# Optimization experiments

Hardware: AMD Instinct MI355X
Metric: run time of the kernel (lower is better)

Reference implementation:

```python
import jax, jax.numpy as jnp
import numpy as np

HID = 256; HEADS = 8; HD = HID // HEADS; GROUPS = 8; CPG = HID // GROUPS
DIMS = [64, 128, 256, 512]; SIZES = [56, 28, 14, 7]; B = 8


def _linear(x, W, b):
    # torch nn.Linear convention: W is [out, in]
    return jnp.einsum('...i,oi->...o', x, W) + b


def _conv1x1(x, W, b):
    return jnp.einsum('bchw,oc->bohw', x, W) + b[None, :, None, None]


def setup_inputs() -> dict:
    key = jax.random.key(0)
    keys = iter(jax.random.split(key, 64))
    def nrm(shape, s=0.02):
        return jax.random.normal(next(keys), shape, dtype=jnp.float32) * s
    inp = {}
    for i, (d, sz) in enumerate(zip(DIMS, SIZES)):
        inp[f'f{i}'] = jax.random.normal(next(keys), (B, d, sz, sz), dtype=jnp.float32)
        inp[f'Wp{i}'] = nrm((HID, d)); inp[f'bp{i}'] = jnp.zeros((HID,), jnp.float32)
    for n, shp in [('Wq', (HID, HID)), ('Wk', (HID, HID)), ('Wv', (HID, HID)), ('Wo', (HID, HID)),
                   ('Wg1', (HID, 2 * HID)), ('Wg2', (HID, HID)), ('Wcp', (HID, HID)),
                   ('Wkg1', (2 * HID, HID)), ('Wkg2', (GROUPS * 9, 2 * HID)),
                   ('Wit', (HID, HID)), ('Wot', (HID, HID))]:
        inp[n] = nrm(shp)
    for n, dim in [('bq', HID), ('bk', HID), ('bv', HID), ('bo', HID), ('bg1', HID), ('bg2', HID),
                   ('bcp', HID), ('bkg1', 2 * HID), ('bkg2', GROUPS * 9), ('bit', HID), ('bot', HID)]:
        inp[n] = jnp.zeros((dim,), jnp.float32)
    inp['gamma'] = jnp.ones((HID,), jnp.float32)
    inp['beta'] = jnp.zeros((HID,), jnp.float32)
    return inp


def reference(f0, f1, f2, f3, Wp0, bp0, Wp1, bp1, Wp2, bp2, Wp3, bp3,
              Wq, bq, Wk, bk, Wv, bv, Wo, bo, Wg1, bg1, Wg2, bg2,
              Wcp, bcp, Wkg1, bkg1, Wkg2, bkg2, Wit, bit, Wot, bot, gamma, beta):
    feats = [f0, f1, f2, f3]
    Wps = [Wp0, Wp1, Wp2, Wp3]; bps = [bp0, bp1, bp2, bp3]
    b = f0.shape[0]
    # ---- ACSA: 1x1 projections to hidden_dim, flatten spatial to tokens ----
    proj = [_conv1x1(f, W, bb) for f, W, bb in zip(feats, Wps, bps)]  # [B,HID,H,W]
    flat = [p.reshape(b, HID, -1).transpose(0, 2, 1) for p in proj]   # [B,S,HID]
    scale = 1.0 / jnp.sqrt(jnp.float32(HD))
    enhanced = []
    for i, xi in enumerate(flat):
        q = _linear(xi, Wq, bq).reshape(b, -1, HEADS, HD).transpose(0, 2, 1, 3)  # [B,H,Si,d]
        e = xi
        for j, xj in enumerate(flat):
            if i == j:
                continue
            k = _linear(xj, Wk, bk).reshape(b, -1, HEADS, HD).transpose(0, 2, 1, 3)
            v = _linear(xj, Wv, bv).reshape(b, -1, HEADS, HD).transpose(0, 2, 1, 3)
            attn = jax.nn.softmax(jnp.einsum('bhqd,bhkd->bhqk', q, k) * scale, axis=-1)
            ctx = jnp.einsum('bhqk,bhkd->bhqd', attn, v).transpose(0, 2, 1, 3).reshape(b, -1, HID)
            ctx = _linear(ctx, Wo, bo)
            gate = jax.nn.sigmoid(_linear(jax.nn.relu(_linear(jnp.concatenate([e, ctx], -1), Wg1, bg1)), Wg2, bg2))
            e = e + gate * ctx
        enhanced.append(e.transpose(0, 2, 1).reshape(b, HID, proj[i].shape[2], proj[i].shape[3]))
    # ---- CECM per scale: dynamic per-sample grouped 3x3 conv ----
    outs = []
    for x in enhanced:
        H, W = x.shape[2], x.shape[3]
        ctx = jax.nn.relu(_linear(x.mean((2, 3)), Wcp, bcp))                       # [B,HID]
        kern = _linear(jax.nn.relu(_linear(ctx, Wkg1, bkg1)), Wkg2, bkg2)          # [B,G*9]
        kern = kern.reshape(b, GROUPS, 3, 3)
        xt = _conv1x1(x, Wit, bit)                                                 # [B,HID,H,W]
        # per-(sample,group) kernel shared across channels within group -> depthwise conv
        kern_rep = jnp.broadcast_to(kern[:, :, None], (b, GROUPS, CPG, 3, 3)).reshape(b * HID, 1, 3, 3)
        y = jax.lax.conv_general_dilated(
            xt.reshape(1, b * HID, H, W), kern_rep, (1, 1), ((1, 1), (1, 1)),
            dimension_numbers=('NCHW', 'OIHW', 'NCHW'), feature_group_count=b * HID
        ).reshape(b, HID, H, W)
        y = _conv1x1(y, Wot, bot)
        # BatchNorm2d (training-mode batch statistics, biased var, eps=1e-5)
        mu = y.mean((0, 2, 3)); var = y.var((0, 2, 3))
        y = (y - mu[None, :, None, None]) * jax.lax.rsqrt(var + 1e-5)[None, :, None, None]
        y = y * gamma[None, :, None, None] + beta[None, :, None, None]
        outs.append((xt + y).reshape(b, HID, -1))
    # concat scales along flattened-spatial axis -> [B, HID, 3136+784+196+49]
    return jnp.concatenate(outs, axis=-1)
```

## Files before the change

### kernel.cpp

```cpp
#include <hip/hip_runtime.h>
#include <hip/hip_bf16.h>
#include <cstddef>

#define NB 8
#define HIDC 256
#define NHEAD 8
#define HDIM 32
#define TTOK 33320
#define STOT 4165
#define VTP 33440
#define QKVS 768
#define QSC2 0.2550348757f
#define BN1_CH 128

static const int H_SZ[4]   = {56, 28, 14, 7};
static const int S_SZ[4]   = {3136, 784, 196, 49};
static const int D_IN[4]   = {64, 128, 256, 512};
static const int BOFF[4]   = {0, 25088, 31360, 32928};
static const int SKPAD_H[4]= {3136, 784, 200, 56};
static const int VWOFF_H[4]= {0, 25088, 31360, 32960};

__constant__ int DC_S[4]     = {3136, 784, 196, 49};
__constant__ int DC_HW[4]    = {56, 28, 14, 7};
__constant__ int DC_BOFF[4]  = {0, 25088, 31360, 32928};
__constant__ int DC_GOFF[4]  = {0, 3136, 3920, 4116};
__constant__ int DC_FOS[4]   = {0, 49, 62, 66};

__constant__ int FP_SQ[12]   = {784,196,49,3136,196,49,3136,784,49,3136,784,196};
__constant__ int FP_SK[12]   = {3136,3136,3136,784,784,784,196,196,196,49,49,49};
__constant__ int FP_QOFF[12] = {25088,31360,32928,0,31360,32928,0,25088,32928,0,25088,31360};
__constant__ int FP_KOFF[12] = {0,0,0,25088,25088,25088,31360,31360,31360,32928,32928,32928};
__constant__ int FP_VOFF[12] = {0,0,0,25088,25088,25088,31360,31360,31360,32960,32960,32960};
__constant__ int FP_SKP[12]  = {3136,3136,3136,784,784,784,200,200,200,56,56,56};
__constant__ int FP_R[12]    = {0,0,0,0,1,1,1,1,2,2,2,2};
__constant__ int FP_SB0[13]  = {0,13,17,18,31,32,33,46,50,51,64,68,69};

typedef short bf16s;
typedef bf16s bf16x8 __attribute__((ext_vector_type(8)));
typedef float f32x4 __attribute__((ext_vector_type(4)));

static __device__ inline bf16s f2b(float f) {
    return (bf16s)((__float_as_uint(f) + 0x8000u) >> 16);
}
static __device__ inline float b2f(bf16s s) {
    return __uint_as_float(((unsigned)(unsigned short)s) << 16);
}
static __device__ inline unsigned cvtpk(float a, float b) {
    unsigned r;
    asm("v_cvt_pk_bf16_f32 %0, %1, %2" : "=v"(r) : "v"(a), "v"(b));
    return r;
}
static __device__ inline float ex2(float x) {
#if __has_builtin(__builtin_amdgcn_exp2f)
    return __builtin_amdgcn_exp2f(x);
#else
    return exp2f(x);
#endif
}
#define MFMA16(a, b, c) __builtin_amdgcn_mfma_f32_16x16x32_bf16(a, b, c, 0, 0, 0)
#define ZERO4 ((f32x4){0.f, 0.f, 0.f, 0.f})

struct CvtArgs {
    const float* src[15];
    void* dst[15];
    int n[15];
    int mode[15];
    int K[15];
};
__global__ __launch_bounds__(256) void cvt_all(CvtArgs a, int total) {
    int idx = blockIdx.x * 256 + threadIdx.x;
    if (idx >= total) return;
    int seg = 0, off = idx;
    while (off >= a.n[seg]) { off -= a.n[seg]; seg++; }
    float v = a.src[seg][off];
    int m = a.mode[seg];
    if (m == 1 || m == 3) v *= QSC2;
    if (m <= 1) {
        int K = a.K[seg];
        int kz = __builtin_ctz(K);
        int n = off >> kz, k = off & (K - 1);
        int c64 = n >> 6, nt = (n >> 4) & 3, l15 = n & 15;
        int k32 = k >> 5, q = (k >> 3) & 3, j = k & 7;
        int dst = (((c64 * (K >> 5) + k32) * 4 + nt) << 9) + l15 * 32 + q * 8 + j;
        ((bf16s*)a.dst[seg])[dst] = f2b(v);
    } else {
        ((float*)a.dst[seg])[off] = v;
    }
}

__global__ __launch_bounds__(256) void transpose_f2(const float* __restrict__ f,
                                                    bf16s* __restrict__ A, int D, int S) {
    __shared__ float t[32][33];
    int s0 = blockIdx.x * 32, d0 = blockIdx.y * 32, b = blockIdx.z;
    int sl = threadIdx.x & 31, dl = threadIdx.x >> 5;
    #pragma unroll
    for (int dd = 0; dd < 32; dd += 8) {
        int s = s0 + sl;
        t[dl + dd][sl] = (s < S) ? f[((size_t)(b * D + d0 + dl + dd)) * S + s] : 0.f;
    }
    __syncthreads();
    int dc = threadIdx.x & 31, sg = threadIdx.x >> 5;
    #pragma unroll
    for (int ss = 0; ss < 32; ss += 8) {
        int s = s0 + sg + ss;
        if (s < S) A[((size_t)(b * S + s)) * D + d0 + dc] = f2b(t[dc][sg + ss]);
    }
}

template <int EPI>
__global__ __launch_bounds__(256) void gemm3(
    const bf16s* __restrict__ A, const bf16s* __restrict__ A2,
    const bf16s* __restrict__ W, const float* __restrict__ bias,
    float* __restrict__ Cf, bf16s* __restrict__ Cb, const bf16s* __restrict__ Gaux,
    int M, int N, int K, int K1)
{
    int tid = threadIdx.x, lane = tid & 63, wave = tid >> 6;
    int l15 = lane & 15, quad = lane >> 4;
    int row0 = blockIdx.y * 64 + (wave >> 1) * 32;
    int col0 = blockIdx.x * 128 + (wave & 1) * 64;
    int K2 = K - K1;
    int nk = K >> 5;
    int c64 = (blockIdx.x << 1) + (wave & 1);
    const bf16s* wbase = W + (size_t)c64 * ((size_t)nk << 11) + l15 * 32 + quad * 8;
    int ra[2];
    #pragma unroll
    for (int mt = 0; mt < 2; mt++) ra[mt] = min(row0 + mt * 16 + l15, M - 1);

    f32x4 acc[2][4];
    #pragma unroll
    for (int i = 0; i < 2; i++)
        #pragma unroll
        for (int j = 0; j < 4; j++) acc[i][j] = ZERO4;

    bf16x8 aA[2], wA[4], aB[2], wB[4];

    auto loadA = [&](bf16x8* af, int k32) {
        int kk = (k32 << 5) + quad * 8;
        if (kk < K1) {
            #pragma unroll
            for (int mt = 0; mt < 2; mt++)
                af[mt] = *(const bf16x8*)(A + (size_t)ra[mt] * K1 + kk);
        } else {
            int k2 = kk - K1;
            #pragma unroll
            for (int mt = 0; mt < 2; mt++)
                af[mt] = *(const bf16x8*)(A2 + (size_t)ra[mt] * K2 + k2);
        }
    };
    auto loadW = [&](bf16x8* wf, int k32) {
        const bf16s* p = wbase + ((size_t)k32 << 11);
        #pragma unroll
        for (int nt = 0; nt < 4; nt++)
            wf[nt] = *(const bf16x8*)(p + nt * 512);
    };

    loadA(aA, 0); loadW(wA, 0);
    for (int k32 = 0; k32 < nk; k32 += 2) {
        loadA(aB, k32 + 1); loadW(wB, k32 + 1);
        #pragma unroll
        for (int mt = 0; mt < 2; mt++)
            #pragma unroll
            for (int nt = 0; nt < 4; nt++)
                acc[mt][nt] = MFMA16(aA[mt], wA[nt], acc[mt][nt]);
        if (k32 + 2 < nk) { loadA(aA, k32 + 2); loadW(wA, k32 + 2); }
        #pragma unroll
        for (int mt = 0; mt < 2; mt++)
            #pragma unroll
            for (int nt = 0; nt < 4; nt++)
                acc[mt][nt] = MFMA16(aB[mt], wB[nt], acc[mt][nt]);
    }

    #pragma unroll
    for (int mt = 0; mt < 2; mt++) {
        int rowb = row0 + mt * 16 + quad * 4;
        #pragma unroll
        for (int nt = 0; nt < 4; nt++) {
            int col = col0 + nt * 16 + l15;
            float bv = bias ? bias[col] : 0.f;
            #pragma unroll
            for (int r = 0; r < 4; r++) {
                int row = rowb + r;
                if (row >= M) continue;
                size_t off = (size_t)row * N + col;
                float v = acc[mt][nt][r] + bv;
                if (EPI == 0) {
                    Cb[off] = f2b(v);
                } else if (EPI == 1) {
                    Cf[off] = v; Cb[off] = f2b(v);
                } else {
                    Cf[off] = v;
                }
            }
        }
    }
}

#define GLDS 264
__global__ __launch_bounds__(256) void gatefuse(
    const bf16s* __restrict__ ctxob, bf16s* __restrict__ xb, const float* __restrict__ x,
    const bf16s* __restrict__ Wg1, const float* __restrict__ bg1,
    const bf16s* __restrict__ Wg2, const float* __restrict__ bg2, int M)
{
    __shared__ bf16s ebf[32 * GLDS], cxb[32 * GLDS], hbf[32 * GLDS];
    int tid = threadIdx.x, lane = tid & 63, wave = tid >> 6;
    int l15 = lane & 15, quad = lane >> 4;
    int r0 = blockIdx.x * 32;
    int col0 = wave * 64;

    #pragma unroll
    for (int u = 0; u < 4; u++) {
        int idx = u * 256 + tid;
        int row = idx >> 5, ch = (idx & 31) * 8;
        *(bf16x8*)&ebf[row * GLDS + ch] =
            *(const bf16x8*)(xb + (size_t)min(r0 + row, M - 1) * HIDC + ch);
    }
    f32x4 e32[2][4];
    #pragma unroll
    for (int mt = 0; mt < 2; mt++)
        #pragma unroll
        for (int nt = 0; nt < 4; nt++)
            #pragma unroll
            for (int rr = 0; rr < 4; rr++) {
                int row = min(r0 + mt * 16 + quad * 4 + rr, M - 1);
                e32[mt][nt][rr] = x[(size_t)row * HIDC + col0 + nt * 16 + l15];
            }

    const bf16s* w1base = Wg1 + ((size_t)wave << 15) + l15 * 32 + quad * 8;
    const bf16s* w2base = Wg2 + ((size_t)wave << 14) + l15 * 32 + quad * 8;

    for (int r = 0; r < 3; r++) {
        __syncthreads();
        const bf16s* crp = ctxob + (size_t)r * ((size_t)TTOK * HIDC);
        #pragma unroll
        for (int u = 0; u < 4; u++) {
            int idx = u * 256 + tid;
            int row = idx >> 5, ch = (idx & 31) * 8;
            *(bf16x8*)&cxb[row * GLDS + ch] =
                *(const bf16x8*)(crp + (size_t)min(r0 + row, M - 1) * HIDC + ch);
        }
        __syncthreads();

        f32x4 acc[2][4];
        bf16x8 aA[2], wA[4], aB[2], wB[4];

        #pragma unroll
        for (int i = 0; i < 2; i++)
            #pragma unroll
            for (int j = 0; j < 4; j++) acc[i][j] = ZERO4;
        auto loadA1 = [&](bf16x8* af, int k32) {
            int kk = (k32 << 5) + quad * 8;
            if (kk < 256) {
                #pragma unroll
                for (int mt = 0; mt < 2; mt++)
                    af[mt] = *(const bf16x8*)&ebf[(mt * 16 + l15) * GLDS + kk];
            } else {
                #pragma unroll
                for (int mt = 0; mt < 2; mt++)
                    af[mt] = *(const bf16x8*)&cxb[(mt * 16 + l15) * GLDS + kk - 256];
            }
        };
        auto loadW1 = [&](bf16x8* wf, int k32) {
            const bf16s* p = w1base + ((size_t)k32 << 11);
            #pragma unroll
            for (int nt = 0; nt < 4; nt++)
                wf[nt] = *(const bf16x8*)(p + nt * 512);
        };
        loadA1(aA, 0); loadW1(wA, 0);
        for (int k32 = 0; k32 < 16; k32 += 2) {
            loadA1(aB, k32 + 1); loadW1(wB, k32 + 1);
            #pragma unroll
            for (int mt = 0; mt < 2; mt++)
                #pragma unroll
                for (int nt = 0; nt < 4; nt++)
                    acc[mt][nt] = MFMA16(aA[mt], wA[nt], acc[mt][nt]);
            if (k32 + 2 < 16) { loadA1(aA, k32 + 2); loadW1(wA, k32 + 2); }
            #pragma unroll
            for (int mt = 0; mt < 2; mt++)
                #pragma unroll
                for (int nt = 0; nt < 4; nt++)
                    acc[mt][nt] = MFMA16(aB[mt], wB[nt], acc[mt][nt]);
        }
        #pragma unroll
        for (int mt = 0; mt < 2; mt++)
            #pragma unroll
            for (int nt = 0; nt < 4; nt++)
                #pragma unroll
                for (int rr = 0; rr < 4; rr++) {
                    int row = mt * 16 + quad * 4 + rr;
                    int col = col0 + nt * 16 + l15;
                    hbf[row * GLDS + col] = f2b(fmaxf(acc[mt][nt][rr] + bg1[col], 0.f));
                }
        __syncthreads();

        #pragma unroll
        for (int i = 0; i < 2; i++)
            #pragma unroll
            for (int j = 0; j < 4; j++) acc[i][j] = ZERO4;
        auto loadA2 = [&](bf16x8* af, int k32) {
            int kk = (k32 << 5) + quad * 8;
            #pragma unroll
            for (int mt = 0; mt < 2; mt++)
                af[mt] = *(const bf16x8*)&hbf[(mt * 16 + l15) * GLDS + kk];
        };
        auto loadW2 = [&](bf16x8* wf, int k32) {
            const bf16s* p = w2base + ((size_t)k32 << 11);
            #pragma unroll
            for (int nt = 0; nt < 4; nt++)
                wf[nt] = *(const bf16x8*)(p + nt * 512);
        };
        loadA2(aA, 0); loadW2(wA, 0);
        for (int k32 = 0; k32 < 8; k32 += 2) {
            loadA2(aB, k32 + 1); loadW2(wB, k32 + 1);
            #pragma unroll
            for (int mt = 0; mt < 2; mt++)
                #pragma unroll
                for (int nt = 0; nt < 4; nt++)
                    acc[mt][nt] = MFMA16(aA[mt], wA[nt], acc[mt][nt]);
            if (k32 + 2 < 8) { loadA2(aA, k32 + 2); loadW2(wA, k32 + 2); }
            #pragma unroll
            for (int mt = 0; mt < 2; mt++)
                #pragma unroll
                for (int nt = 0; nt < 4; nt++)
                    acc[mt][nt] = MFMA16(aB[mt], wB[nt], acc[mt][nt]);
        }
        #pragma unroll
        for (int mt = 0; mt < 2; mt++)
            #pragma unroll
            for (int nt = 0; nt < 4; nt++)
                #pragma unroll
                for (int rr = 0; rr < 4; rr++) {
                    int row = mt * 16 + quad * 4 + rr;
                    int col = col0 + nt * 16 + l15;
                    float v = acc[mt][nt][rr] + bg2[col];
                    float g = 1.f / (1.f + __expf(-v));
                    e32[mt][nt][rr] += g * b2f(cxb[row * GLDS + col]);
                }
        if (r < 2) {
            #pragma unroll
            for (int mt = 0; mt < 2; mt++)
                #pragma unroll
                for (int nt = 0; nt < 4; nt++)
                    #pragma unroll
                    for (int rr = 0; rr < 4; rr++) {
                        int row = mt * 16 + quad * 4 + rr;
                        int col = col0 + nt * 16 + l15;
                        ebf[row * GLDS + col] = f2b(e32[mt][nt][rr]);
                    }
        }
    }

    #pragma unroll
    for (int mt = 0; mt < 2; mt++)
        #pragma unroll
        for (int nt = 0; nt < 4; nt++)
            #pragma unroll
            for (int rr = 0; rr < 4; rr++) {
                int row = r0 + mt * 16 + quad * 4 + rr;
                if (row < M)
                    xb[(size_t)row * HIDC + col0 + nt * 16 + l15] = f2b(e32[mt][nt][rr]);
            }
}

__global__ __launch_bounds__(256) void transpose_v(const bf16s* __restrict__ vsrc,
                                                   bf16s* __restrict__ vdst,
                                                   int Mtok, int Sk, int SkPad, int voff, int VS) {
    __shared__ bf16s t[64][72];
    int t0 = blockIdx.x * 64, d0 = blockIdx.y * 64;
    int tid = threadIdx.x;
    int lr = tid >> 2, lc = (tid & 3) * 16;
    if (t0 + lr < Mtok) {
        bf16x8 v0 = *(const bf16x8*)(vsrc + (size_t)(t0 + lr) * VS + d0 + lc);
        bf16x8 v1 = *(const bf16x8*)(vsrc + (size_t)(t0 + lr) * VS + d0 + lc + 8);
        *(bf16x8*)&t[lr][lc] = v0;
        *(bf16x8*)&t[lr][lc + 8] = v1;
    }
    __syncthreads();
    int dr = tid >> 2, tc = (tid & 3) * 16;
    #pragma unroll
    for (int u = 0; u < 16; u++) {
        int tok = t0 + tc + u;
        if (tok >= Mtok) break;
        int bidx = tok / Sk, s = tok - bidx * Sk;
        vdst[(size_t)(d0 + dr) * VTP + voff + bidx * SkPad + s] = t[tc + u][dr];
    }
}

__global__ __launch_bounds__(256) void flash8(const bf16s* __restrict__ qkv,
                                              const bf16s* __restrict__ vtb,
                                              bf16s* __restrict__ ctxall)
{
    __shared__ bf16s L[4][64 * 40];
    __shared__ float CMB[3][16][64];
    __shared__ float CLS[3][4][64];
    int bx = blockIdx.x;
    int sbg = bx >> 6, hb = bx & 63;
    int h = hb & 7, b = hb >> 3;
    int p = 0;
    while (sbg >= FP_SB0[p + 1]) p++;
    int wave = threadIdx.x >> 6, lane = threadIdx.x & 63;
    int l15 = lane & 15, quad = lane >> 4;
    int Sq = FP_SQ[p], Sk = FP_SK[p];
    bool ksp = (p < 3);
    int qrow0 = ksp ? (sbg - FP_SB0[p]) * 64
                    : ((sbg - FP_SB0[p]) * 4 + wave) * 64;
    if (qrow0 >= Sq) return;
    int k0 = ksp ? wave * 784 : 0;
    int klim = ksp ? 784 : Sk;
    int qoff = FP_QOFF[p], koff = FP_KOFF[p];
    int voff = FP_VOFF[p], skp = FP_SKP[p];
    bf16s* ctxr = ctxall + (size_t)FP_R[p] * TTOK * HIDC;

    const bf16s* qrow = qkv + (size_t)(qoff + b * Sq) * QKVS + h * HDIM + quad * 8;
    bf16x8 qf[4];
    #pragma unroll
    for (int qi = 0; qi < 4; qi++)
        qf[qi] = *(const bf16x8*)(qrow + (size_t)min(qrow0 + qi * 16 + l15, Sq - 1) * QKVS);

    const bf16s* kp0 = qkv + 256 + (size_t)(koff + b * Sk + k0 + l15) * QKVS + h * HDIM + quad * 8;
    const bf16s* kp16 = kp0 + (size_t)16 * QKVS;
    const bf16s* vp0 = vtb + (size_t)(h * HDIM + l15) * VTP + voff + b * skp + k0 + quad * 8;
    const bf16s* vp16 = vp0 + (size_t)16 * VTP;
    bf16s* Lw = L[wave];

    f32x4 a0[4], a1[4];
    float ls[4];
    #pragma unroll
    for (int qi = 0; qi < 4; qi++) { a0[qi] = ZERO4; a1[qi] = ZERO4; ls[qi] = 0.f; }
    int niter = (klim + 31) >> 5;

    bf16x8 kA0, kA1, vA0, vA1, kB0, kB1, vB0, vB1;

    auto loadKV = [&](bf16x8& kf0, bf16x8& kf1, bf16x8& vf0, bf16x8& vf1, int t) {
        size_t kb = (size_t)(t << 5) * QKVS;
        kf0 = *(const bf16x8*)(kp0 + kb);
        kf1 = *(const bf16x8*)(kp16 + kb);
        vf0 = *(const bf16x8*)(vp0 + (t << 5));
        vf1 = *(const bf16x8*)(vp16 + (t << 5));
    };
    auto compute = [&](bf16x8 kf0, bf16x8 kf1, bf16x8 vf0, bf16x8 vf1, int t) {
        int kt = t << 5;
        f32x4 s0[4], s1[4];
        #pragma unroll
        for (int qi = 0; qi < 4; qi++) {
            s0[qi] = MFMA16(kf0, qf[qi], ZERO4);
            s1[qi] = MFMA16(kf1, qf[qi], ZERO4);
        }
        float p0[4][4], p1[4][4];
        #pragma unroll
        for (int qi = 0; qi < 4; qi++)
            #pragma unroll
            for (int r = 0; r < 4; r++) {
                p0[qi][r] = ex2(s0[qi][r]);
                p1[qi][r] = ex2(s1[qi][r]);
            }
        if (kt + 32 > klim) {
            int lim0 = klim - kt - quad * 4, lim1 = lim0 - 16;
            #pragma unroll
            for (int qi = 0; qi < 4; qi++)
                #pragma unroll
                for (int r = 0; r < 4; r++) {
                    if (r >= lim0) p0[qi][r] = 0.f;
                    if (r >= lim1) p1[qi][r] = 0.f;
                }
        }
        #pragma unroll
        for (int qi = 0; qi < 4; qi++) {
            #pragma unroll
            for (int r = 0; r < 4; r++) ls[qi] += p0[qi][r] + p1[qi][r];
            *(uint2*)&Lw[(qi * 16 + l15) * 40 + quad * 4] =
                make_uint2(cvtpk(p0[qi][0], p0[qi][1]), cvtpk(p0[qi][2], p0[qi][3]));
            *(uint2*)&Lw[(qi * 16 + l15) * 40 + 16 + quad * 4] =
                make_uint2(cvtpk(p1[qi][0], p1[qi][1]), cvtpk(p1[qi][2], p1[qi][3]));
        }
        #pragma unroll
        for (int qi = 0; qi < 4; qi++) {
            bf16x8 pb = *(const bf16x8*)&Lw[(qi * 16 + l15) * 40 + quad * 8];
            a0[qi] = MFMA16(vf0, pb, a0[qi]);
            a1[qi] = MFMA16(vf1, pb, a1[qi]);
        }
    };

    loadKV(kA0, kA1, vA0, vA1, 0);
    for (int t = 0; t < niter; t += 2) {
        if (t + 1 < niter) loadKV(kB0, kB1, vB0, vB1, t + 1);
        compute(kA0, kA1, vA0, vA1, t);
        if (t + 2 < niter) loadKV(kA0, kA1, vA0, vA1, t + 2);
        if (t + 1 < niter) compute(kB0, kB1, vB0, vB1, t + 1);
    }

    if (ksp) {
        if (wave > 0) {
            #pragma unroll
            for (int qi = 0; qi < 4; qi++) {
                #pragma unroll
                for (int r = 0; r < 4; r++) CMB[wave - 1][qi * 4 + r][lane] = a0[qi][r];
                CLS[wave - 1][qi][lane] = ls[qi];
            }
        }
        __syncthreads();
        if (wave == 0) {
            #pragma unroll
            for (int w = 0; w < 3; w++)
                #pragma unroll
                for (int qi = 0; qi < 4; qi++) {
                    #pragma unroll
                    for (int r = 0; r < 4; r++) a0[qi][r] += CMB[w][qi * 4 + r][lane];
                    ls[qi] += CLS[w][qi][lane];
                }
        }
        __syncthreads();
        if (wave > 0) {
            #pragma unroll
            for (int qi = 0; qi < 4; qi++)
                #pragma unroll
                for (int r = 0; r < 4; r++) CMB[wave - 1][qi * 4 + r][lane] = a1[qi][r];
        }
        __syncthreads();
        if (wave > 0) return;
        #pragma unroll
        for (int w = 0; w < 3; w++)
            #pragma unroll
            for (int qi = 0; qi < 4; qi++)
                #pragma unroll
                for (int r = 0; r < 4; r++) a1[qi][r] += CMB[w][qi * 4 + r][lane];
    }

    #pragma unroll
    for (int qi = 0; qi < 4; qi++) {
        float l = ls[qi];
        l += __shfl_xor(l, 16); l += __shfl_xor(l, 32);
        float inv = 1.f / l;
        if (qrow0 + qi * 16 + l15 < Sq) {
            size_t o = (size_t)(qoff + b * Sq + qrow0 + qi * 16 + l15) * HIDC + h * HDIM;
            *(uint2*)(ctxr + o + quad * 4) =
                make_uint2(cvtpk(a0[qi][0] * inv, a0[qi][1] * inv),
                           cvtpk(a0[qi][2] * inv, a0[qi][3] * inv));
            *(uint2*)(ctxr + o + 16 + quad * 4) =
                make_uint2(cvtpk(a1[qi][0] * inv, a1[qi][1] * inv),
                           cvtpk(a1[qi][2] * inv, a1[qi][3] * inv));
        }
    }
}

__global__ __launch_bounds__(256) void pool2(const bf16s* __restrict__ xb,
                                             float* __restrict__ partial) {
    int chunk = blockIdx.x, b = blockIdx.y, i = blockIdx.z;
    int c = threadIdx.x;
    int S = DC_S[i];
    int len = (S + 31) / 32;
    int s0 = chunk * len, s1 = min(S, s0 + len);
    float acc = 0.f;
    const bf16s* base = xb + (size_t)(DC_BOFF[i] + b * S) * HIDC + c;
    for (int s = s0; s < s1; s++) acc += b2f(base[(size_t)s * HIDC]);
    partial[(size_t)((i * NB + b) * 32 + chunk) * HIDC + c] = acc;
}

__global__ __launch_bounds__(256) void kgen2(
    const float* __restrict__ partial,
    const float* __restrict__ Wcp, const float* __restrict__ bcp,
    const float* __restrict__ Wkg1, const float* __restrict__ bkg1,
    const float* __restrict__ Wkg2, const float* __restrict__ bkg2,
    float* __restrict__ kern)
{
    __shared__ float pl[256], cv[256], h1[512];
    int b = blockIdx.x, i = blockIdx.y, t = threadIdx.x;
    float invS = 1.f / (float)DC_S[i];
    const float* pb = partial + (size_t)((i * NB + b) * 32) * HIDC;
    float s = 0.f;
    for (int jc = 0; jc < 32; jc++) s += pb[(size_t)jc * HIDC + t];
    pl[t] = s * invS;
    __syncthreads();
    float a = bcp[t];
    for (int k = 0; k < 256; k++) a += Wcp[t * 256 + k] * pl[k];
    cv[t] = fmaxf(a, 0.f);
    __syncthreads();
    for (int r = t; r < 512; r += 256) {
        float a2 = bkg1[r];
        for (int k = 0; k < 256; k++) a2 += Wkg1[r * 256 + k] * cv[k];
        h1[r] = fmaxf(a2, 0.f);
    }
    __syncthreads();
    if (t < 72) {
        float a3 = bkg2[t];
        for (int k = 0; k < 512; k++) a3 += Wkg2[t * 512 + k] * h1[k];
        kern[(i * NB + b) * 72 + t] = a3;
    }
}

__global__ __launch_bounds__(256) void dwconv2(const bf16s* __restrict__ xtb,
                                               const float* __restrict__ kern,
                                               bf16s* __restrict__ y) {
    int tok = blockIdx.x;
    int i = (tok >= DC_BOFF[1]) + (tok >= DC_BOFF[2]) + (tok >= DC_BOFF[3]);
    int S = DC_S[i], W = DC_HW[i];
    int local = tok - DC_BOFF[i];
    int b = local / S, s = local - b * S;
    int hh = s / W, ww = s - hh * W;
    int c = threadIdx.x;
    const float* kb = kern + (i * NB + b) * 72 + (c >> 5) * 9;
    const bf16s* xbase = xtb + (size_t)(DC_BOFF[i] + b * S) * HIDC + c;
    float acc = 0.f;
    #pragma unroll
    for (int ky = 0; ky < 3; ky++) {
        int hy = hh + ky - 1;
        if (hy < 0 || hy >= W) continue;
        #pragma unroll
        for (int kx = 0; kx < 3; kx++) {
            int wx = ww + kx - 1;
            if (wx < 0 || wx >= W) continue;
            acc += kb[ky * 3 + kx] * b2f(xbase[(size_t)(hy * W + wx) * HIDC]);
        }
    }
    y[(size_t)tok * HIDC + c] = f2b(acc);
}

__global__ __launch_bounds__(256) void bn1(const float* __restrict__ yo,
                                           float* __restrict__ bnp) {
    __shared__ float red[4][64][8];
    int chunk = blockIdx.x, i = blockIdx.y, t = threadIdx.x;
    int rg = t >> 6, cq = (t & 63) * 4;
    int Nrows = NB * DC_S[i];
    const float* base = yo + (size_t)DC_BOFF[i] * HIDC + cq;
    f32x4 s = ZERO4, ss = ZERO4;
    for (int r = chunk * 4 + rg; r < Nrows; r += BN1_CH * 4) {
        f32x4 v = *(const f32x4*)(base + (size_t)r * HIDC);
        s += v; ss += v * v;
    }
    #pragma unroll
    for (int j = 0; j < 4; j++) { red[rg][t & 63][j] = s[j]; red[rg][t & 63][4 + j] = ss[j]; }
    __syncthreads();
    if (t < 64) {
        #pragma unroll
        for (int j = 0; j < 4; j++) {
            float a = red[0][t][j] + red[1][t][j] + red[2][t][j] + red[3][t][j];
            float b = red[0][t][4 + j] + red[1][t][4 + j] + red[2][t][4 + j] + red[3][t][4 + j];
            bnp[(size_t)(i * BN1_CH + chunk) * 512 + t * 4 + j] = a;
            bnp[(size_t)(i * BN1_CH + chunk) * 512 + 256 + t * 4 + j] = b;
        }
    }
}
__global__ __launch_bounds__(256) void bn2(const float* __restrict__ bnp,
                                           float* __restrict__ stat) {
    int i = blockIdx.x, c = threadIdx.x;
    float s = 0.f, ss = 0.f;
    for (int ch = 0; ch < BN1_CH; ch++) {
        s += bnp[(size_t)(i * BN1_CH + ch) * 512 + c];
        ss += bnp[(size_t)(i * BN1_CH + ch) * 512 + 256 + c];
    }
    float inv = 1.f / (float)(NB * DC_S[i]);
    float mu = s * inv;
    float var = fmaxf(ss * inv - mu * mu, 0.f);
    stat[i * 512 + c] = mu;
    stat[i * 512 + 256 + c] = rsqrtf(var + 1e-5f);
}

__global__ __launch_bounds__(256) void final2(const bf16s* __restrict__ xtb,
                                              const float* __restrict__ yo,
                                              const float* __restrict__ stat,
                                              const float* __restrict__ gamma,
                                              const float* __restrict__ beta,
                                              float* __restrict__ out) {
    __shared__ float tile[64][65];
    int bx = blockIdx.x;
    int i = (bx >= DC_FOS[1]) + (bx >= DC_FOS[2]) + (bx >= DC_FOS[3]);
    int S = DC_S[i];
    int s0 = (bx - DC_FOS[i]) * 64;
    int cstrip = blockIdx.y, b = blockIdx.z;
    int g = threadIdx.x >> 6, sl = threadIdx.x & 63;
    {
        int c = cstrip * 64 + sl;
        float mu = stat[i * 512 + c], rstd = stat[i * 512 + 256 + c];
        float ga = gamma[c], be = beta[c];
        size_t rbase = (size_t)(DC_BOFF[i] + b * S) * HIDC + c;
        #pragma unroll
        for (int u = 0; u < 16; u++) {
            int s = s0 + g * 16 + u;
            if (s < S) {
                size_t r = rbase + (size_t)s * HIDC;
                tile[g * 16 + u][sl] = b2f(xtb[r]) + (yo[r] - mu) * rstd * ga + be;
            }
        }
    }
    __syncthreads();
    {
        int s = s0 + sl;
        if (s < S) {
            #pragma unroll
            for (int cs = 0; cs < 16; cs++) {
                int cl = g * 16 + cs;
                out[((size_t)(b * HIDC + cstrip * 64 + cl)) * STOT + DC_GOFF[i] + s] = tile[sl][cl];
            }
        }
    }
}

static inline void gemm_launch(hipStream_t st, const bf16s* A, const bf16s* A2,
                               const bf16s* W, const float* bias,
                               float* Cf, bf16s* Cb, const bf16s* Gaux,
                               int M, int N, int K, int K1, int epi) {
    dim3 grid(N / 128, (M + 63) / 64), blk(256);
    switch (epi) {
        case 0: gemm3<0><<<grid, blk, 0, st>>>(A, A2, W, bias, Cf, Cb, Gaux, M, N, K, K1); break;
        case 1: gemm3<1><<<grid, blk, 0, st>>>(A, A2, W, bias, Cf, Cb, Gaux, M, N, K, K1); break;
        default: gemm3<4><<<grid, blk, 0, st>>>(A, A2, W, bias, Cf, Cb, Gaux, M, N, K, K1); break;
    }
}

extern "C" void kernel_launch(void* const* d_in, const int* in_sizes, int n_in,
                              void* d_out, int out_size, void* d_ws, size_t ws_size,
                              hipStream_t stream) {
    typedef const float* fp;
    fp f[4]  = {(fp)d_in[0], (fp)d_in[3], (fp)d_in[6], (fp)d_in[9]};
    fp Wp[4] = {(fp)d_in[1], (fp)d_in[4], (fp)d_in[7], (fp)d_in[10]};
    fp bp[4] = {(fp)d_in[2], (fp)d_in[5], (fp)d_in[8], (fp)d_in[11]};
    fp Wq = (fp)d_in[12], Wk = (fp)d_in[13], Wv = (fp)d_in[14], Wo = (fp)d_in[15];
    fp Wg1 = (fp)d_in[16], Wg2 = (fp)d_in[17], Wcp = (fp)d_in[18];
    fp Wkg1 = (fp)d_in[19], Wkg2 = (fp)d_in[20], Wit = (fp)d_in[21], Wot = (fp)d_in[22];
    fp bq = (fp)d_in[23], bk = (fp)d_in[24], bv = (fp)d_in[25], bo = (fp)d_in[26];
    fp bg1 = (fp)d_in[27], bg2 = (fp)d_in[28], bcp = (fp)d_in[29];
    fp bkg1 = (fp)d_in[30], bkg2 = (fp)d_in[31], bit = (fp)d_in[32], bot = (fp)d_in[33];
    fp gamma = (fp)d_in[34], beta = (fp)d_in[35];
    float* out = (float*)d_out;

    const size_t NT = (size_t)TTOK * HIDC;

    float* x     = (float*)d_ws;
    bf16s* xb    = (bf16s*)(x + NT);
    bf16s* qkvb  = xb + NT;
    bf16s* vtb   = qkvb + (size_t)TTOK * QKVS;
    bf16s* ctxall= vtb + (size_t)HIDC * VTP;
    bf16s* ctxob = ctxall + 3 * NT;
    float* partial = (float*)(ctxob + 3 * NT);
    float* kern    = partial + 4 * NB * 32 * HIDC;
    float* bnp     = kern + 4 * NB * 72;
    float* bnstat  = bnp + 4 * 32 * 512;
    float* bqkv    = bnstat + 4 * 512;
    bf16s* wseg    = (bf16s*)(bqkv + 768);
    bf16s* atmp = ctxall;
    bf16s* hb   = ctxall;
    bf16s* xtb  = ctxall + NT;
    float* yo   = x;
    float* bnp2 = partial;

    bf16s* wpb[4]; size_t wo_ = 0;
    for (int i = 0; i < 4; i++) { wpb[i] = wseg + wo_; wo_ += (size_t)HIDC * D_IN[i]; }
    bf16s* wqkvb = wseg + wo_; wo_ += (size_t)QKVS * 256;
    bf16s* wob  = wseg + wo_; wo_ += 65536;
    bf16s* wg1b = wseg + wo_; wo_ += 131072;
    bf16s* wg2b = wseg + wo_; wo_ += 65536;
    bf16s* witb = wseg + wo_; wo_ += 65536;
    bf16s* wotb = wseg + wo_; wo_ += 65536;

    {
        CvtArgs ca;
        const float* srcs[15] = {Wp[0], Wp[1], Wp[2], Wp[3], Wq, Wk, Wv, Wo, Wg1, Wg2,
                                 Wit, Wot, bq, bk, bv};
        void* dsts[15] = {wpb[0], wpb[1], wpb[2], wpb[3], wqkvb, wqkvb + 65536,
                          wqkvb + 131072, wob, wg1b, wg2b, witb, wotb,
                          bqkv, bqkv + 256, bqkv + 512};
        int ns[15] = {16384, 32768, 65536, 131072, 65536, 65536, 65536, 65536, 131072,
                      65536, 65536, 65536, 256, 256, 256};
        int modes[15] = {0, 0, 0, 0, 1, 0, 0, 0, 0, 0, 0, 0, 3, 2, 2};
        int Ks[15] = {64, 128, 256, 512, 256, 256, 256, 256, 512, 256, 256, 256, 0, 0, 0};
        int total = 0;
        for (int k = 0; k < 15; k++) { ca.src[k] = srcs[k]; ca.dst[k] = dsts[k];
                                       ca.n[k] = ns[k]; ca.mode[k] = modes[k];
                                       ca.K[k] = Ks[k]; total += ns[k]; }
        cvt_all<<<dim3((total + 255) / 256), dim3(256), 0, stream>>>(ca, total);
    }
    hipMemsetAsync(vtb, 0, (size_t)HIDC * VTP * sizeof(bf16s), stream);

    for (int i = 0; i < 4; i++) {
        int S = S_SZ[i], D = D_IN[i], M = NB * S;
        transpose_f2<<<dim3((S + 31) / 32, D / 32, NB), dim3(256), 0, stream>>>(f[i], atmp, D, S);
        gemm_launch(stream, atmp, nullptr, wpb[i], bp[i],
                    x + (size_t)BOFF[i] * HIDC, xb + (size_t)BOFF[i] * HIDC, nullptr,
                    M, HIDC, D, D, 1);
    }

    gemm_launch(stream, xb, nullptr, wqkvb, bqkv, nullptr, qkvb, nullptr, TTOK, QKVS, 256, 256, 0);
    for (int j = 0; j < 4; j++) {
        int Mtok = NB * S_SZ[j];
        transpose_v<<<dim3((Mtok + 63) / 64, 4), dim3(256), 0, stream>>>(
            qkvb + 512 + (size_t)BOFF[j] * QKVS, vtb, Mtok, S_SZ[j], SKPAD_H[j], VWOFF_H[j], QKVS);
    }

    flash8<<<dim3(69 * 64), dim3(256), 0, stream>>>(qkvb, vtb, ctxall);
    gemm_launch(stream, ctxall, nullptr, wob, bo, nullptr, ctxob, nullptr, 3 * TTOK, HIDC, 256, 256, 0);
    gatefuse<<<dim3((TTOK + 31) / 32), dim3(256), 0, stream>>>(
        ctxob, xb, x, wg1b, bg1, wg2b, bg2, TTOK);

    pool2<<<dim3(32, NB, 4), dim3(256), 0, stream>>>(xb, partial);
    kgen2<<<dim3(NB, 4), dim3(256), 0, stream>>>(partial, Wcp, bcp, Wkg1, bkg1, Wkg2, bkg2, kern);
    gemm_launch(stream, xb, nullptr, witb, bit, nullptr, xtb, nullptr, TTOK, HIDC, 256, 256, 0);
    dwconv2<<<dim3(TTOK), dim3(256), 0, stream>>>(xtb, kern, hb);
    gemm_launch(stream, hb, nullptr, wotb, bot, yo, nullptr, nullptr, TTOK, HIDC, 256, 256, 4);
    bn1<<<dim3(BN1_CH, 4), dim3(256), 0, stream>>>(yo, bnp2);
    bn2<<<dim3(4), dim3(256), 0, stream>>>(bnp2, bnstat);
    final2<<<dim3(67, 4, NB), dim3(256), 0, stream>>>(xtb, yo, bnstat, gamma, beta, out);
}
```

Measured before the change: 850.4 us.

## Fuse output projection into gate kernel and repack K per head

The separate GEMM for the attention output projection (Wo) is removed. It is now computed inside the gatefuse kernel per 32-row tile from ctxall, with the result staged in shared memory before the gate MLP. A new kpack kernel also rearranges K into a head-major contiguous layout so flash attention loads K tiles with unit stride instead of strided QKV rows. This saves a full round trip of the 3x ctx output through global memory, at the cost of an extra pack pass and more work and syncs in gatefuse.

After: 920.8 us. 1.08x slower.

```diff
diff --git a/kernel.cpp b/kernel.cpp
--- a/kernel.cpp
+++ b/kernel.cpp
@@ -195,9 +195,20 @@
     }
 }
 
+__global__ __launch_bounds__(256) void kpack(const bf16s* __restrict__ qkvK,
+                                             bf16s* __restrict__ ktb) {
+    int tid = threadIdx.x;
+    int tok = blockIdx.x * 8 + (tid >> 5);
+    if (tok >= TTOK) return;
+    int ch = (tid & 31) * 8;
+    bf16x8 v = *(const bf16x8*)(qkvK + (size_t)tok * QKVS + ch);
+    *(bf16x8*)(ktb + ((size_t)(ch >> 5) * TTOK + tok) * 32 + (ch & 31)) = v;
+}
+
 #define GLDS 264
 __global__ __launch_bounds__(256) void gatefuse(
-    const bf16s* __restrict__ ctxob, bf16s* __restrict__ xb, const float* __restrict__ x,
+    const bf16s* __restrict__ ctxall, bf16s* __restrict__ xb, const float* __restrict__ x,
+    const bf16s* __restrict__ Wo, const float* __restrict__ bo,
     const bf16s* __restrict__ Wg1, const float* __restrict__ bg1,
     const bf16s* __restrict__ Wg2, const float* __restrict__ bg2, int M)
 {
@@ -225,23 +236,67 @@
                 e32[mt][nt][rr] = x[(size_t)row * HIDC + col0 + nt * 16 + l15];
             }
 
+    const bf16s* wobase = Wo + ((size_t)wave << 14) + l15 * 32 + quad * 8;
     const bf16s* w1base = Wg1 + ((size_t)wave << 15) + l15 * 32 + quad * 8;
     const bf16s* w2base = Wg2 + ((size_t)wave << 14) + l15 * 32 + quad * 8;
 
     for (int r = 0; r < 3; r++) {
         __syncthreads();
-        const bf16s* crp = ctxob + (size_t)r * ((size_t)TTOK * HIDC);
+        const bf16s* crp = ctxall + (size_t)r * ((size_t)TTOK * HIDC);
         #pragma unroll
         for (int u = 0; u < 4; u++) {
             int idx = u * 256 + tid;
             int row = idx >> 5, ch = (idx & 31) * 8;
-            *(bf16x8*)&cxb[row * GLDS + ch] =
+            *(bf16x8*)&hbf[row * GLDS + ch] =
                 *(const bf16x8*)(crp + (size_t)min(r0 + row, M - 1) * HIDC + ch);
         }
         __syncthreads();
 
         f32x4 acc[2][4];
         bf16x8 aA[2], wA[4], aB[2], wB[4];
+
+        #pragma unroll
+        for (int i = 0; i < 2; i++)
+            #pragma unroll
+            for (int j = 0; j < 4; j++) acc[i][j] = ZERO4;
+        auto loadAo = [&](bf16x8* af, int k32) {
+            int kk = (k32 << 5) + quad * 8;
+            #pragma unroll
+            for (int mt = 0; mt < 2; mt++)
+                af[mt] = *(const bf16x8*)&hbf[(mt * 16 + l15) * GLDS + kk];
+        };
+        auto loadWo = [&](bf16x8* wf, int k32) {
+            const bf16s* p = wobase + ((size_t)k32 << 11);
+            #pragma unroll
+            for (int nt = 0; nt < 4; nt++)
+                wf[nt] = *(const bf16x8*)(p + nt * 512);
+        };
+        loadAo(aA, 0); loadWo(wA, 0);
+        for (int k32 = 0; k32 < 8; k32 += 2) {
+            loadAo(aB, k32 + 1); loadWo(wB, k32 + 1);
+            #pragma unroll
+            for (int mt = 0; mt < 2; mt++)
+                #pragma unroll
+                for (int nt = 0; nt < 4; nt++)
+                    acc[mt][nt] = MFMA16(aA[mt], wA[nt], acc[mt][nt]);
+            if (k32 + 2 < 8) { loadAo(aA, k32 + 2); loadWo(wA, k32 + 2); }
+            #pragma unroll
+            for (int mt = 0; mt < 2; mt++)
+                #pragma unroll
+                for (int nt = 0; nt < 4; nt++)
+                    acc[mt][nt] = MFMA16(aB[mt], wB[nt], acc[mt][nt]);
+        }
+        #pragma unroll
+        for (int mt = 0; mt < 2; mt++)
+            #pragma unroll
+            for (int nt = 0; nt < 4; nt++)
+                #pragma unroll
+                for (int rr = 0; rr < 4; rr++) {
+                    int row = mt * 16 + quad * 4 + rr;
+                    int col = col0 + nt * 16 + l15;
+                    cxb[row * GLDS + col] = f2b(acc[mt][nt][rr] + bo[col]);
+                }
+        __syncthreads();
 
         #pragma unroll
         for (int i = 0; i < 2; i++)
@@ -280,6 +335,7 @@
                 for (int nt = 0; nt < 4; nt++)
                     acc[mt][nt] = MFMA16(aB[mt], wB[nt], acc[mt][nt]);
         }
+        __syncthreads();
         #pragma unroll
         for (int mt = 0; mt < 2; mt++)
             #pragma unroll
@@ -387,6 +443,7 @@
 
 __global__ __launch_bounds__(256) void flash8(const bf16s* __restrict__ qkv,
                                               const bf16s* __restrict__ vtb,
+                                              const bf16s* __restrict__ ktb,
                                               bf16s* __restrict__ ctxall)
 {
     __shared__ bf16s L[4][64 * 40];
@@ -416,9 +473,9 @@
     for (int qi = 0; qi < 4; qi++)
         qf[qi] = *(const bf16x8*)(qrow + (size_t)min(qrow0 + qi * 16 + l15, Sq - 1) * QKVS);
 
-    const bf16s* kp0 = qkv + 256 + (size_t)(koff + b * Sk + k0 + l15) * QKVS + h * HDIM + quad * 8;
-    const bf16s* kp16 = kp0 + (size_t)16 * QKVS;
-    const bf16s* vp0 = vtb + (size_t)(h * HDIM + l15) * VTP + voff + b * skp + k0 + quad * 8;
+    const bf16s* kp0 = ktb + ((size_t)h * TTOK + koff + b * Sk + k0 + l15) * 32 + quad * 8;
+    const bf16s* kp16 = kp0 + 512;
+    const bf16s* vp0 = vtb + (size_t)(h * HDIM + l15) * VTP + voff + b * skp + quad * 8;
     const bf16s* vp16 = vp0 + (size_t)16 * VTP;
     bf16s* Lw = L[wave];
 
@@ -431,11 +488,11 @@
     bf16x8 kA0, kA1, vA0, vA1, kB0, kB1, vB0, vB1;
 
     auto loadKV = [&](bf16x8& kf0, bf16x8& kf1, bf16x8& vf0, bf16x8& vf1, int t) {
-        size_t kb = (size_t)(t << 5) * QKVS;
+        size_t kb = (size_t)t << 10;
         kf0 = *(const bf16x8*)(kp0 + kb);
         kf1 = *(const bf16x8*)(kp16 + kb);
-        vf0 = *(const bf16x8*)(vp0 + (t << 5));
-        vf1 = *(const bf16x8*)(vp16 + (t << 5));
+        vf0 = *(const bf16x8*)(vp0 + k0 + (t << 5));
+        vf1 = *(const bf16x8*)(vp16 + k0 + (t << 5));
     };
     auto compute = [&](bf16x8 kf0, bf16x8 kf1, bf16x8 vf0, bf16x8 vf1, int t) {
         int kt = t << 5;
@@ -741,6 +798,7 @@
     bf16s* xtb  = ctxall + NT;
     float* yo   = x;
     float* bnp2 = partial;
+    bf16s* ktb  = ctxob;
 
     bf16s* wpb[4]; size_t wo_ = 0;
     for (int i = 0; i < 4; i++) { wpb[i] = wseg + wo_; wo_ += (size_t)HIDC * D_IN[i]; }
@@ -784,11 +842,11 @@
         transpose_v<<<dim3((Mtok + 63) / 64, 4), dim3(256), 0, stream>>>(
             qkvb + 512 + (size_t)BOFF[j] * QKVS, vtb, Mtok, S_SZ[j], SKPAD_H[j], VWOFF_H[j], QKVS);
     }
-
-    flash8<<<dim3(69 * 64), dim3(256), 0, stream>>>(qkvb, vtb, ctxall);
-    gemm_launch(stream, ctxall, nullptr, wob, bo, nullptr, ctxob, nullptr, 3 * TTOK, HIDC, 256, 256, 0);
+    kpack<<<dim3((TTOK + 7) / 8), dim3(256), 0, stream>>>(qkvb + 256, ktb);
+
+    flash8<<<dim3(69 * 64), dim3(256), 0, stream>>>(qkvb, vtb, ktb, ctxall);
     gatefuse<<<dim3((TTOK + 31) / 32), dim3(256), 0, stream>>>(
-        ctxob, xb, x, wg1b, bg1, wg2b, bg2, TTOK);
+        ctxall, xb, x, wob, bo, wg1b, bg1, wg2b, bg2, TTOK);
 
     pool2<<<dim3(32, NB, 4), dim3(256), 0, stream>>>(xb, partial);
     kgen2<<<dim3(NB, 4), dim3(256), 0, stream>>>(partial, Wcp, bcp, Wkg1, bkg1, Wkg2, bkg2, kern);
```
